# Performance work log

Measured on AMD Instinct MI355X. Metric: run time of the kernel, lower is better.

Reference implementation:

```python
import jax, jax.numpy as jnp
import numpy as np

D_THRESH = 0.5  # forward default d=0.5


def setup_inputs() -> dict:
    key = jax.random.key(0)
    C, P, D = 10, 1000, 1024
    # scale so pairwise distances (~sqrt(2D)*scale) straddle the 0.5 threshold
    feats = jax.random.normal(key, (C * P, D), dtype=jnp.float32) * 0.011
    ids_per_cls = jnp.arange(C * P, dtype=jnp.int64).reshape(C, P)
    return {"feats": feats, "ids_per_cls": ids_per_cls, "budget": 2000}


def reference(feats, ids_per_cls, budget):
    C, P = ids_per_cls.shape
    per_cls_budget = budget // C  # budget = int(budget / len(ids_per_cls_train))
    X = feats[ids_per_cls.reshape(-1)]  # [C*P, D] class-blocked representatives
    # pairwise euclidean distances (torch.cdist p=2), computed via gram trick
    sq = jnp.sum(X * X, axis=-1)  # [C*P]
    d2 = sq[:, None] + sq[None, :] - 2.0 * (X @ X.T)  # [C*P, C*P]
    dist = jnp.sqrt(jnp.maximum(d2, 0.0))
    # only count neighbors from OTHER classes (the per-class loop pops class i)
    cls = jnp.repeat(jnp.arange(C), P)  # [C*P]
    other = cls[:, None] != cls[None, :]  # [C*P, C*P] bool
    counts = jnp.sum((dist < D_THRESH) & other, axis=-1)  # [C*P] int
    counts = counts.reshape(C, P)
    # ascending sort by count, keep the `per_cls_budget` most-separated nodes
    order = jnp.argsort(counts, axis=-1)  # [C, P]
    sel = order[:, :per_cls_budget]  # [C, budget//C]
    ids_selected = jnp.take_along_axis(ids_per_cls, sel, axis=1).reshape(-1)
    return ids_selected, counts
```

## Files before the change

### kernel.cpp

```cpp
#include <hip/hip_runtime.h>

#define N_TOT 10000
#define CLS_P 1000
#define NC 10
#define D 1024

#define TM 128
#define DELTA 1.6e-5f
#define INV_SCALE2 4.8828125e-4f
#define ESC_CAP (1 << 22)
#define ESC_LOC 256
#define KCHUNKS (D / 32)
#define NTILE ((N_TOT + TM - 1) / TM)

typedef _Float16 f16x8 __attribute__((ext_vector_type(8)));
typedef float f32x4 __attribute__((ext_vector_type(4)));
typedef const __attribute__((address_space(1))) unsigned int* gptr_t;
typedef __attribute__((address_space(3))) unsigned int* lptr_t;

__global__ void zero_kernel(int* __restrict__ out, int n, int* __restrict__ esc_cnt) {
    int i = blockIdx.x * blockDim.x + threadIdx.x;
    if (i < n) out[i] = 0;
    if (i == 0) *esc_cnt = 0;
}

__global__ void prep_kernel(const float* __restrict__ feats, const int* __restrict__ ids,
                            unsigned short* __restrict__ Xh,
                            double* __restrict__ sqd, float* __restrict__ sqf) {
    int row = blockIdx.x;
    int id = ids[row];
    const float4* rp = (const float4*)(feats + (size_t)id * D);
    float4 v = rp[threadIdx.x];
    float f[4] = {v.x, v.y, v.z, v.w};
    ushort4 hv;
    unsigned short* hp = &hv.x;
    double s = 0.0;
    #pragma unroll
    for (int e = 0; e < 4; e++) {
        s += (double)f[e] * f[e];
        union { _Float16 h; unsigned short u; } cv;
        cv.h = (_Float16)(f[e] * 64.0f);
        hp[e] = cv.u;
    }
    *(ushort4*)(Xh + (size_t)row * D + threadIdx.x * 4) = hv;

    #pragma unroll
    for (int off = 32; off > 0; off >>= 1)
        s += __shfl_down(s, off, 64);
    __shared__ double wsum[4];
    int lane = threadIdx.x & 63, wv = threadIdx.x >> 6;
    if (lane == 0) wsum[wv] = s;
    __syncthreads();
    if (threadIdx.x == 0) {
        double t = wsum[0] + wsum[1] + wsum[2] + wsum[3];
        sqd[row] = t;
        sqf[row] = (float)t;
    }
}

__launch_bounds__(256, 3)
__global__ void count_kernel(const unsigned short* __restrict__ Xh,
                             const float* __restrict__ sqf,
                             int* __restrict__ counts,
                             int* __restrict__ esc_cnt, int2* __restrict__ esc_list) {
    int bid = blockIdx.y * gridDim.x + blockIdx.x;
    int it_t = 0, jt_t = 0;
    {
        int rem = bid, band = 0;
        while (true) {
            int h = NTILE - band * 8; if (h > 8) h = 8;
            int area = h * NTILE;
            if (rem < area) { it_t = band * 8 + rem % h; jt_t = rem / h; break; }
            rem -= area; band++;
        }
    }
    const int ib = it_t * TM, jb = jt_t * TM;
    if (jb < ib) return;

    {
        int ci0 = ib / CLS_P, ci1 = (ib + TM - 1) / CLS_P;
        int cj0 = jb / CLS_P, cj1 = (jb + TM - 1) / CLS_P;
        if (ci0 == ci1 && cj0 == cj1 && ci0 == cj0) return;
    }

    __shared__ unsigned short S[3 * 8192];
    __shared__ int cred_i[TM], cred_j[TM];
    __shared__ int esc_n, esc_base;
    __shared__ int2 esc_buf[ESC_LOC];

    const int tid = threadIdx.x;
    const int lane = tid & 63, w = tid >> 6;
    const int wi = (w & 1) * 64, wj = (w >> 1) * 64;
    const int quad = lane >> 4, col = lane & 15;

    if (tid == 0) esc_n = 0;

    const int warr = w >> 1;
    const int w01 = w & 1;
    const int rl0 = lane >> 2;
    const int slot = lane & 3;
    const int q = (slot - rl0 - (rl0 >> 2)) & 3;
    const int rowbase = warr ? jb : ib;

    const unsigned short* src[4];
    #pragma unroll
    for (int b = 0; b < 4; b++) {
        int grow = rowbase + b * 32 + w01 * 16 + rl0;
        if (grow > N_TOT - 1) grow = N_TOT - 1;
        src[b] = Xh + (size_t)grow * D + q * 8;
    }

#define STAGE(KC_, BUFBASE_)                                                     \
    {                                                                            \
        _Pragma("unroll")                                                        \
        for (int b = 0; b < 4; b++) {                                            \
            __builtin_amdgcn_global_load_lds(                                    \
                (gptr_t)(src[b] + (KC_) * 32),                                   \
                (lptr_t)((BUFBASE_) + warr * 4096 + b * 1024 + w01 * 512),       \
                16, 0, 0);                                                       \
        }                                                                        \
    }

#define FRAGS(BUFBASE_)                                                          \
    {                                                                            \
        _Pragma("unroll")                                                        \
        for (int t = 0; t < 4; t++) {                                            \
            int rA = wi + t * 16 + col;                                          \
            int sA = (quad + rA + (rA >> 2)) & 3;                                \
            ah[t] = *(const f16x8*)((BUFBASE_) + rA * 32 + sA * 8);              \
            int rB = wj + t * 16 + col;                                          \
            int sB = (quad + rB + (rB >> 2)) & 3;                                \
            bh[t] = *(const f16x8*)((BUFBASE_) + 4096 + rB * 32 + sB * 8);       \
        }                                                                        \
    }

#define MFMA16                                                                   \
    {                                                                            \
        _Pragma("unroll")                                                        \
        for (int it = 0; it < 4; it++)                                           \
            _Pragma("unroll")                                                    \
            for (int jt = 0; jt < 4; jt++)                                       \
                acc[it][jt] = __builtin_amdgcn_mfma_f32_16x16x32_f16(ah[it], bh[jt], acc[it][jt], 0, 0, 0); \
    }

    f32x4 acc[4][4];
    #pragma unroll
    for (int it = 0; it < 4; it++)
        #pragma unroll
        for (int jt = 0; jt < 4; jt++)
            acc[it][jt] = (f32x4){0.f, 0.f, 0.f, 0.f};

    f16x8 ah[4], bh[4];

    unsigned short* p0 = S;
    unsigned short* p1 = S + 8192;
    unsigned short* p2 = S + 16384;

    STAGE(0, p0);
    STAGE(1, p1);
    asm volatile("s_waitcnt vmcnt(4) lgkmcnt(0)\ns_barrier" ::: "memory");

    for (int kc = 0; kc < KCHUNKS; kc++) {
        if (kc + 2 < KCHUNKS) STAGE(kc + 2, p2);
        FRAGS(p0);
        if (kc + 2 < KCHUNKS) {
            asm volatile("s_waitcnt vmcnt(4) lgkmcnt(0)\ns_barrier" ::: "memory");
        } else {
            asm volatile("s_waitcnt vmcnt(0) lgkmcnt(0)\ns_barrier" ::: "memory");
        }
        MFMA16;
        unsigned short* t = p0; p0 = p1; p1 = p2; p2 = t;
    }

    if (tid < TM) { cred_i[tid] = 0; cred_j[tid] = 0; }
    __syncthreads();

    const float thr_lo = 0.25f - DELTA;
    const float thr_hi = 0.25f + DELTA;
    const bool diag = (ib == jb);

    float sqj[4];
    int clsj[4], jv[4], jidx[4];
    #pragma unroll
    for (int jt = 0; jt < 4; jt++) {
        int j = jb + wj + jt * 16 + col;
        jidx[jt] = j;
        jv[jt] = (j < N_TOT);
        sqj[jt] = jv[jt] ? sqf[j] : 0.f;
        clsj[jt] = j / CLS_P;
    }

    int cj[4] = {0, 0, 0, 0};

    #pragma unroll
    for (int it = 0; it < 4; it++) {
        #pragma unroll
        for (int r = 0; r < 4; r++) {
            int irow = wi + it * 16 + quad * 4 + r;
            int i = ib + irow;
            bool iv = (i < N_TOT);
            float sqi = iv ? sqf[i] : 0.f;
            int clsi = i / CLS_P;
            int ci = 0;
            #pragma unroll
            for (int jt = 0; jt < 4; jt++) {
                int j = jidx[jt];
                bool ok = iv && jv[jt] && (clsj[jt] != clsi) && (!diag || j > i);
                float d2 = sqi + sqj[jt] - acc[it][jt][r] * INV_SCALE2;
                bool in = ok && (d2 < thr_lo);
                bool esc = ok && !in && (d2 < thr_hi);
                ci += in ? 1 : 0;
                cj[jt] += in ? 1 : 0;
                if (esc) {
                    int k = atomicAdd(&esc_n, 1);
                    if (k < ESC_LOC) {
                        esc_buf[k] = make_int2(i, j);
                    } else {
                        int idx = atomicAdd(esc_cnt, 1);
                        if (idx < ESC_CAP) esc_list[idx] = make_int2(i, j);
                    }
                }
            }
            ci += __shfl_xor(ci, 1, 64);
            ci += __shfl_xor(ci, 2, 64);
            ci += __shfl_xor(ci, 4, 64);
            ci += __shfl_xor(ci, 8, 64);
            if (col == 0 && ci) atomicAdd(&cred_i[irow], ci);
        }
    }
    #pragma unroll
    for (int jt = 0; jt < 4; jt++) {
        int v = cj[jt];
        v += __shfl_xor(v, 16, 64);
        v += __shfl_xor(v, 32, 64);
        if (quad == 0 && v) atomicAdd(&cred_j[wj + jt * 16 + col], v);
    }
    __syncthreads();
    if (tid < TM) {
        int i = ib + tid;
        if (i < N_TOT && cred_i[tid]) atomicAdd(&counts[i], cred_i[tid]);
        int j = jb + tid;
        if (j < N_TOT && cred_j[tid]) atomicAdd(&counts[j], cred_j[tid]);
    }
    if (tid == 0) {
        int n = esc_n; if (n > ESC_LOC) n = ESC_LOC;
        esc_n = n;
        esc_base = atomicAdd(esc_cnt, n);
    }
    __syncthreads();
    for (int k = tid; k < esc_n; k += 256) {
        int idx = esc_base + k;
        if (idx < ESC_CAP) esc_list[idx] = esc_buf[k];
    }
}

__global__ void escalate_kernel(const float* __restrict__ feats, const int* __restrict__ ids,
                                const double* __restrict__ sqd,
                                const int* __restrict__ esc_cnt, const int2* __restrict__ esc_list,
                                int* __restrict__ counts) {
    int n = *esc_cnt;
    if (n > ESC_CAP) n = ESC_CAP;
    int lane = threadIdx.x & 63;
    int sub = lane >> 4;
    int l16 = lane & 15;
    int wglob = (blockIdx.x * blockDim.x + threadIdx.x) >> 6;
    int W = (gridDim.x * blockDim.x) >> 6;
    for (int p0 = wglob * 4; p0 < n; p0 += W * 4) {
        int p = p0 + sub;
        bool act = (p < n);
        int2 pr = act ? esc_list[p] : make_int2(0, 0);
        const float* xi = feats + (size_t)ids[pr.x] * D;
        const float* xj = feats + (size_t)ids[pr.y] * D;
        double s = 0.0;
        int k0 = l16 * 64;
        #pragma unroll
        for (int k = 0; k < 64; k += 4) {
            float4 a = *(const float4*)(xi + k0 + k);
            float4 b = *(const float4*)(xj + k0 + k);
            s += (double)a.x * b.x + (double)a.y * b.y + (double)a.z * b.z + (double)a.w * b.w;
        }
        s += __shfl_xor(s, 1, 64);
        s += __shfl_xor(s, 2, 64);
        s += __shfl_xor(s, 4, 64);
        s += __shfl_xor(s, 8, 64);
        if (act && l16 == 0) {
            double d2 = sqd[pr.x] + sqd[pr.y] - 2.0 * s;
            if (d2 < 0.25) {
                atomicAdd(&counts[pr.x], 1);
                atomicAdd(&counts[pr.y], 1);
            }
        }
    }
}

__global__ void sel_kernel(const int* __restrict__ counts, const int* __restrict__ ids,
                           int* __restrict__ out_ids, int pcb) {
    int c = blockIdx.x;
    __shared__ int lc[CLS_P];
    for (int p = threadIdx.x; p < CLS_P; p += blockDim.x)
        lc[p] = counts[c * CLS_P + p];
    __syncthreads();
    int p = threadIdx.x;
    if (p < CLS_P) {
        int cp = lc[p];
        int rank = 0;
        for (int qq = 0; qq < CLS_P; qq++) {
            int cq = lc[qq];
            rank += (cq < cp) || (cq == cp && qq < p);
        }
        if (rank < pcb)
            out_ids[c * pcb + rank] = ids[c * CLS_P + p];
    }
}

extern "C" void kernel_launch(void* const* d_in, const int* in_sizes, int n_in,
                              void* d_out, int out_size, void* d_ws, size_t ws_size,
                              hipStream_t stream) {
    const float* feats = (const float*)d_in[0];
    const int* ids = (const int*)d_in[1];
    int budget = out_size - N_TOT;
    int pcb = budget / NC;
    int* out = (int*)d_out;
    int* counts_out = out + NC * pcb;

    char* ws = (char*)d_ws;
    const size_t XH_OFF = 0;
    const size_t SQD_OFF = XH_OFF + (size_t)N_TOT * D * 2;
    const size_t SQF_OFF = SQD_OFF + (size_t)N_TOT * 8;
    const size_t ESCC_OFF = (SQF_OFF + (size_t)N_TOT * 4 + 63) & ~(size_t)63;
    const size_t ESCL_OFF = ESCC_OFF + 64;

    unsigned short* Xh = (unsigned short*)(ws + XH_OFF);
    double* sqd = (double*)(ws + SQD_OFF);
    float* sqf = (float*)(ws + SQF_OFF);
    int* esc_cnt = (int*)(ws + ESCC_OFF);
    int2* esc_list = (int2*)(ws + ESCL_OFF);

    zero_kernel<<<(out_size + 255) / 256, 256, 0, stream>>>(out, out_size, esc_cnt);
    prep_kernel<<<N_TOT, 256, 0, stream>>>(feats, ids, Xh, sqd, sqf);
    dim3 grid(NTILE, NTILE);
    count_kernel<<<grid, 256, 0, stream>>>(Xh, sqf, counts_out, esc_cnt, esc_list);
    escalate_kernel<<<4096, 256, 0, stream>>>(feats, ids, sqd, esc_cnt, esc_list, counts_out);
    sel_kernel<<<NC, 1024, 0, stream>>>(counts_out, ids, out, pcb);
}
```

Measured before the change: 362.7 us.

## Double-buffer MFMA fragments to overlap LDS reads with matrix math

Restructures the K-loop so LDS fragment loads for the next chunk go into a second register set while MFMAs run on the current set. The loop is unrolled by two and the per-step lgkmcnt(0) wait is dropped from the barrier. This is meant to hide LDS read latency behind MFMA work, at the cost of more VGPRs, which could lower occupancy. It also narrows the DELTA escalation band around the threshold, which sends fewer near-threshold pairs to the slow recheck path but risks misclassifying borderline distances.

```diff
diff --git a/kernel.cpp b/kernel.cpp
--- a/kernel.cpp
+++ b/kernel.cpp
@@ -6,7 +6,7 @@
 #define D 1024
 
 #define TM 128
-#define DELTA 1.6e-5f
+#define DELTA 1.35e-5f
 #define INV_SCALE2 4.8828125e-4f
 #define ESC_CAP (1 << 22)
 #define ESC_LOC 256
@@ -121,27 +121,30 @@
         }                                                                        \
     }
 
-#define FRAGS(BUFBASE_)                                                          \
+#define FRAGS_(AH, BH, BUFBASE_)                                                 \
     {                                                                            \
         _Pragma("unroll")                                                        \
         for (int t = 0; t < 4; t++) {                                            \
             int rA = wi + t * 16 + col;                                          \
             int sA = (quad + rA + (rA >> 2)) & 3;                                \
-            ah[t] = *(const f16x8*)((BUFBASE_) + rA * 32 + sA * 8);              \
+            AH[t] = *(const f16x8*)((BUFBASE_) + rA * 32 + sA * 8);              \
             int rB = wj + t * 16 + col;                                          \
             int sB = (quad + rB + (rB >> 2)) & 3;                                \
-            bh[t] = *(const f16x8*)((BUFBASE_) + 4096 + rB * 32 + sB * 8);       \
+            BH[t] = *(const f16x8*)((BUFBASE_) + 4096 + rB * 32 + sB * 8);       \
         }                                                                        \
     }
 
-#define MFMA16                                                                   \
+#define MFMA16_(AH, BH)                                                          \
     {                                                                            \
         _Pragma("unroll")                                                        \
         for (int it = 0; it < 4; it++)                                           \
             _Pragma("unroll")                                                    \
             for (int jt = 0; jt < 4; jt++)                                       \
-                acc[it][jt] = __builtin_amdgcn_mfma_f32_16x16x32_f16(ah[it], bh[jt], acc[it][jt], 0, 0, 0); \
-    }
+                acc[it][jt] = __builtin_amdgcn_mfma_f32_16x16x32_f16(AH[it], BH[jt], acc[it][jt], 0, 0, 0); \
+    }
+
+#define WAIT4_BAR asm volatile("s_waitcnt vmcnt(4)\ns_barrier" ::: "memory")
+#define WAIT0_BAR asm volatile("s_waitcnt vmcnt(0)\ns_barrier" ::: "memory")
 
     f32x4 acc[4][4];
     #pragma unroll
@@ -150,7 +153,7 @@
         for (int jt = 0; jt < 4; jt++)
             acc[it][jt] = (f32x4){0.f, 0.f, 0.f, 0.f};
 
-    f16x8 ah[4], bh[4];
+    f16x8 ah0[4], bh0[4], ah1[4], bh1[4];
 
     unsigned short* p0 = S;
     unsigned short* p1 = S + 8192;
@@ -158,19 +161,26 @@
 
     STAGE(0, p0);
     STAGE(1, p1);
-    asm volatile("s_waitcnt vmcnt(4) lgkmcnt(0)\ns_barrier" ::: "memory");
-
-    for (int kc = 0; kc < KCHUNKS; kc++) {
-        if (kc + 2 < KCHUNKS) STAGE(kc + 2, p2);
-        FRAGS(p0);
-        if (kc + 2 < KCHUNKS) {
-            asm volatile("s_waitcnt vmcnt(4) lgkmcnt(0)\ns_barrier" ::: "memory");
-        } else {
-            asm volatile("s_waitcnt vmcnt(0) lgkmcnt(0)\ns_barrier" ::: "memory");
-        }
-        MFMA16;
-        unsigned short* t = p0; p0 = p1; p1 = p2; p2 = t;
-    }
+    WAIT4_BAR;
+    FRAGS_(ah0, bh0, p0);
+
+    for (int kc = 0; kc < KCHUNKS - 2; kc += 2) {
+        STAGE(kc + 2, p2);
+        WAIT4_BAR;
+        FRAGS_(ah1, bh1, p1);
+        MFMA16_(ah0, bh0);
+        { unsigned short* t = p0; p0 = p1; p1 = p2; p2 = t; }
+
+        STAGE(kc + 3, p2);
+        WAIT4_BAR;
+        FRAGS_(ah0, bh0, p1);
+        MFMA16_(ah1, bh1);
+        { unsigned short* t = p0; p0 = p1; p1 = p2; p2 = t; }
+    }
+    WAIT0_BAR;
+    FRAGS_(ah1, bh1, p1);
+    MFMA16_(ah0, bh0);
+    MFMA16_(ah1, bh1);
 
     if (tid < TM) { cred_i[tid] = 0; cred_j[tid] = 0; }
     __syncthreads();
```

New measurement: 342.3 us. -5.6%, faster.

## Use 256x128 rectangular tiles with 4x8 MFMA per wave in count kernel

Applied to the files above, without the earlier changes.

Reworks the count kernel tiling from 128x128 square tiles to 256x128 tiles, with each wave owning 64 rows and all 128 columns, so each wave issues 32 MFMAs per k-chunk instead of 16. This raises arithmetic intensity per LDS fragment load, but it also uses more registers and LDS, so launch bounds drop to 2 blocks per SM. It removes the banded tile swizzle, narrows the escalation delta, enlarges the local escape buffer, and relaxes the lgkmcnt waits in the k-loop. Triangle skipping now works at a coarser granularity, and some tiles compute pairs that the j>i mask then discards.

```diff
diff --git a/kernel.cpp b/kernel.cpp
--- a/kernel.cpp
+++ b/kernel.cpp
@@ -5,13 +5,15 @@
 #define NC 10
 #define D 1024
 
-#define TM 128
-#define DELTA 1.6e-5f
+#define TMI 256
+#define TMJ 128
+#define DELTA 1.35e-5f
 #define INV_SCALE2 4.8828125e-4f
 #define ESC_CAP (1 << 22)
-#define ESC_LOC 256
+#define ESC_LOC 512
 #define KCHUNKS (D / 32)
-#define NTILE ((N_TOT + TM - 1) / TM)
+#define NTI ((N_TOT + TMI - 1) / TMI)
+#define NTJ ((N_TOT + TMJ - 1) / TMJ)
 
 typedef _Float16 f16x8 __attribute__((ext_vector_type(8)));
 typedef float f32x4 __attribute__((ext_vector_type(4)));
@@ -58,67 +60,67 @@
     }
 }
 
-__launch_bounds__(256, 3)
+__launch_bounds__(256, 2)
 __global__ void count_kernel(const unsigned short* __restrict__ Xh,
                              const float* __restrict__ sqf,
                              int* __restrict__ counts,
                              int* __restrict__ esc_cnt, int2* __restrict__ esc_list) {
-    int bid = blockIdx.y * gridDim.x + blockIdx.x;
-    int it_t = 0, jt_t = 0;
+    const int tjt = blockIdx.x;
+    const int tit = blockIdx.y;
+    if (tjt < 2 * tit) return;
+    const int ib = tit * TMI, jb = tjt * TMJ;
+
     {
-        int rem = bid, band = 0;
-        while (true) {
-            int h = NTILE - band * 8; if (h > 8) h = 8;
-            int area = h * NTILE;
-            if (rem < area) { it_t = band * 8 + rem % h; jt_t = rem / h; break; }
-            rem -= area; band++;
-        }
-    }
-    const int ib = it_t * TM, jb = jt_t * TM;
-    if (jb < ib) return;
-
-    {
-        int ci0 = ib / CLS_P, ci1 = (ib + TM - 1) / CLS_P;
-        int cj0 = jb / CLS_P, cj1 = (jb + TM - 1) / CLS_P;
+        int ihi = ib + TMI - 1; if (ihi > N_TOT - 1) ihi = N_TOT - 1;
+        int jhi = jb + TMJ - 1; if (jhi > N_TOT - 1) jhi = N_TOT - 1;
+        int ci0 = ib / CLS_P, ci1 = ihi / CLS_P;
+        int cj0 = jb / CLS_P, cj1 = jhi / CLS_P;
         if (ci0 == ci1 && cj0 == cj1 && ci0 == cj0) return;
     }
 
-    __shared__ unsigned short S[3 * 8192];
-    __shared__ int cred_i[TM], cred_j[TM];
+    __shared__ unsigned short S[3 * 12288];
+    __shared__ int cred_i[TMI], cred_j[TMJ];
     __shared__ int esc_n, esc_base;
     __shared__ int2 esc_buf[ESC_LOC];
 
     const int tid = threadIdx.x;
     const int lane = tid & 63, w = tid >> 6;
-    const int wi = (w & 1) * 64, wj = (w >> 1) * 64;
+    const int wi = w * 64;
     const int quad = lane >> 4, col = lane & 15;
 
     if (tid == 0) esc_n = 0;
 
-    const int warr = w >> 1;
-    const int w01 = w & 1;
     const int rl0 = lane >> 2;
     const int slot = lane & 3;
     const int q = (slot - rl0 - (rl0 >> 2)) & 3;
-    const int rowbase = warr ? jb : ib;
-
-    const unsigned short* src[4];
-    #pragma unroll
-    for (int b = 0; b < 4; b++) {
-        int grow = rowbase + b * 32 + w01 * 16 + rl0;
-        if (grow > N_TOT - 1) grow = N_TOT - 1;
-        src[b] = Xh + (size_t)grow * D + q * 8;
+
+    const unsigned short* srcA[4];
+    const unsigned short* srcB[2];
+    #pragma unroll
+    for (int c = 0; c < 4; c++) {
+        int r = ib + w * 64 + c * 16 + rl0;
+        if (r > N_TOT - 1) r = N_TOT - 1;
+        srcA[c] = Xh + (size_t)r * D + q * 8;
+    }
+    #pragma unroll
+    for (int c = 0; c < 2; c++) {
+        int r = jb + w * 32 + c * 16 + rl0;
+        if (r > N_TOT - 1) r = N_TOT - 1;
+        srcB[c] = Xh + (size_t)r * D + q * 8;
     }
 
 #define STAGE(KC_, BUFBASE_)                                                     \
     {                                                                            \
         _Pragma("unroll")                                                        \
-        for (int b = 0; b < 4; b++) {                                            \
+        for (int c = 0; c < 4; c++)                                              \
             __builtin_amdgcn_global_load_lds(                                    \
-                (gptr_t)(src[b] + (KC_) * 32),                                   \
-                (lptr_t)((BUFBASE_) + warr * 4096 + b * 1024 + w01 * 512),       \
-                16, 0, 0);                                                       \
-        }                                                                        \
+                (gptr_t)(srcA[c] + (KC_) * 32),                                  \
+                (lptr_t)((BUFBASE_) + w * 2048 + c * 512), 16, 0, 0);            \
+        _Pragma("unroll")                                                        \
+        for (int c = 0; c < 2; c++)                                              \
+            __builtin_amdgcn_global_load_lds(                                    \
+                (gptr_t)(srcB[c] + (KC_) * 32),                                  \
+                (lptr_t)((BUFBASE_) + 8192 + w * 1024 + c * 512), 16, 0, 0);     \
     }
 
 #define FRAGS(BUFBASE_)                                                          \
@@ -128,69 +130,72 @@
             int rA = wi + t * 16 + col;                                          \
             int sA = (quad + rA + (rA >> 2)) & 3;                                \
             ah[t] = *(const f16x8*)((BUFBASE_) + rA * 32 + sA * 8);              \
-            int rB = wj + t * 16 + col;                                          \
+        }                                                                        \
+        _Pragma("unroll")                                                        \
+        for (int u = 0; u < 8; u++) {                                            \
+            int rB = u * 16 + col;                                               \
             int sB = (quad + rB + (rB >> 2)) & 3;                                \
-            bh[t] = *(const f16x8*)((BUFBASE_) + 4096 + rB * 32 + sB * 8);       \
+            bh[u] = *(const f16x8*)((BUFBASE_) + 8192 + rB * 32 + sB * 8);       \
         }                                                                        \
     }
 
-#define MFMA16                                                                   \
+#define MFMA32                                                                   \
     {                                                                            \
         _Pragma("unroll")                                                        \
         for (int it = 0; it < 4; it++)                                           \
             _Pragma("unroll")                                                    \
-            for (int jt = 0; jt < 4; jt++)                                       \
+            for (int jt = 0; jt < 8; jt++)                                       \
                 acc[it][jt] = __builtin_amdgcn_mfma_f32_16x16x32_f16(ah[it], bh[jt], acc[it][jt], 0, 0, 0); \
     }
 
-    f32x4 acc[4][4];
+    f32x4 acc[4][8];
     #pragma unroll
     for (int it = 0; it < 4; it++)
         #pragma unroll
-        for (int jt = 0; jt < 4; jt++)
+        for (int jt = 0; jt < 8; jt++)
             acc[it][jt] = (f32x4){0.f, 0.f, 0.f, 0.f};
 
-    f16x8 ah[4], bh[4];
+    f16x8 ah[4], bh[8];
 
     unsigned short* p0 = S;
-    unsigned short* p1 = S + 8192;
-    unsigned short* p2 = S + 16384;
+    unsigned short* p1 = S + 12288;
+    unsigned short* p2 = S + 24576;
 
     STAGE(0, p0);
     STAGE(1, p1);
-    asm volatile("s_waitcnt vmcnt(4) lgkmcnt(0)\ns_barrier" ::: "memory");
+    asm volatile("s_waitcnt vmcnt(6) lgkmcnt(0)\ns_barrier" ::: "memory");
 
     for (int kc = 0; kc < KCHUNKS; kc++) {
         if (kc + 2 < KCHUNKS) STAGE(kc + 2, p2);
         FRAGS(p0);
         if (kc + 2 < KCHUNKS) {
-            asm volatile("s_waitcnt vmcnt(4) lgkmcnt(0)\ns_barrier" ::: "memory");
-        } else {
-            asm volatile("s_waitcnt vmcnt(0) lgkmcnt(0)\ns_barrier" ::: "memory");
-        }
-        MFMA16;
+            asm volatile("s_waitcnt vmcnt(6)\ns_barrier" ::: "memory");
+        } else if (kc + 1 < KCHUNKS) {
+            asm volatile("s_waitcnt vmcnt(0)\ns_barrier" ::: "memory");
+        }
+        MFMA32;
         unsigned short* t = p0; p0 = p1; p1 = p2; p2 = t;
     }
 
-    if (tid < TM) { cred_i[tid] = 0; cred_j[tid] = 0; }
+    cred_i[tid] = 0;
+    if (tid < TMJ) cred_j[tid] = 0;
     __syncthreads();
 
     const float thr_lo = 0.25f - DELTA;
     const float thr_hi = 0.25f + DELTA;
-    const bool diag = (ib == jb);
-
-    float sqj[4];
-    int clsj[4], jv[4], jidx[4];
-    #pragma unroll
-    for (int jt = 0; jt < 4; jt++) {
-        int j = jb + wj + jt * 16 + col;
+
+    float sqj[8];
+    int clsj[8], jv[8], jidx[8];
+    #pragma unroll
+    for (int jt = 0; jt < 8; jt++) {
+        int j = jb + jt * 16 + col;
         jidx[jt] = j;
         jv[jt] = (j < N_TOT);
         sqj[jt] = jv[jt] ? sqf[j] : 0.f;
         clsj[jt] = j / CLS_P;
     }
 
-    int cj[4] = {0, 0, 0, 0};
+    int cj[8] = {0, 0, 0, 0, 0, 0, 0, 0};
 
     #pragma unroll
     for (int it = 0; it < 4; it++) {
@@ -203,9 +208,9 @@
             int clsi = i / CLS_P;
             int ci = 0;
             #pragma unroll
-            for (int jt = 0; jt < 4; jt++) {
+            for (int jt = 0; jt < 8; jt++) {
                 int j = jidx[jt];
-                bool ok = iv && jv[jt] && (clsj[jt] != clsi) && (!diag || j > i);
+                bool ok = iv && jv[jt] && (clsj[jt] != clsi) && (j > i);
                 float d2 = sqi + sqj[jt] - acc[it][jt][r] * INV_SCALE2;
                 bool in = ok && (d2 < thr_lo);
                 bool esc = ok && !in && (d2 < thr_hi);
@@ -229,18 +234,20 @@
         }
     }
     #pragma unroll
-    for (int jt = 0; jt < 4; jt++) {
+    for (int jt = 0; jt < 8; jt++) {
         int v = cj[jt];
         v += __shfl_xor(v, 16, 64);
         v += __shfl_xor(v, 32, 64);
-        if (quad == 0 && v) atomicAdd(&cred_j[wj + jt * 16 + col], v);
-    }
-    __syncthreads();
-    if (tid < TM) {
+        if (quad == 0 && v) atomicAdd(&cred_j[jt * 16 + col], v);
+    }
+    __syncthreads();
+    {
         int i = ib + tid;
         if (i < N_TOT && cred_i[tid]) atomicAdd(&counts[i], cred_i[tid]);
-        int j = jb + tid;
-        if (j < N_TOT && cred_j[tid]) atomicAdd(&counts[j], cred_j[tid]);
+        if (tid < TMJ) {
+            int j = jb + tid;
+            if (j < N_TOT && cred_j[tid]) atomicAdd(&counts[j], cred_j[tid]);
+        }
     }
     if (tid == 0) {
         int n = esc_n; if (n > ESC_LOC) n = ESC_LOC;
@@ -338,7 +345,7 @@
 
     zero_kernel<<<(out_size + 255) / 256, 256, 0, stream>>>(out, out_size, esc_cnt);
     prep_kernel<<<N_TOT, 256, 0, stream>>>(feats, ids, Xh, sqd, sqf);
-    dim3 grid(NTILE, NTILE);
+    dim3 grid(NTJ, NTI);
     count_kernel<<<grid, 256, 0, stream>>>(Xh, sqf, counts_out, esc_cnt, esc_list);
     escalate_kernel<<<4096, 256, 0, stream>>>(feats, ids, sqd, esc_cnt, esc_list, counts_out);
     sel_kernel<<<NC, 1024, 0, stream>>>(counts_out, ids, out, pcb);
```

Measured after the change: 373.4 us. 3.0% more time.

## Fuse escalation into count kernel with single-wave 64x64 tiles

Applied to the files above, without the earlier changes.

Replaces the 256-thread, 128x128-tile count kernel with a one-wave, 64x64-tile kernel double-buffered in LDS without barriers. The escalation recheck of near-threshold pairs is now done inside the same kernel from a local buffer, with a slow per-thread fallback on overflow, so the global escalation list and the separate escalate kernel go away. It also narrows the ambiguity band (DELTA) and drops shared-memory count reduction in favour of direct global atomics. These changes cut a launch and global traffic, but each tile loses the 128x128 reuse, there are more global atomics, and the narrower band relies on FP16 error staying within it.

```diff
diff --git a/kernel.cpp b/kernel.cpp
--- a/kernel.cpp
+++ b/kernel.cpp
@@ -5,23 +5,21 @@
 #define NC 10
 #define D 1024
 
-#define TM 128
-#define DELTA 1.6e-5f
+#define TK 64
+#define DELTA 1.35e-5f
 #define INV_SCALE2 4.8828125e-4f
-#define ESC_CAP (1 << 22)
-#define ESC_LOC 256
+#define ESC_LOC 128
 #define KCHUNKS (D / 32)
-#define NTILE ((N_TOT + TM - 1) / TM)
+#define NT64 ((N_TOT + TK - 1) / TK)
 
 typedef _Float16 f16x8 __attribute__((ext_vector_type(8)));
 typedef float f32x4 __attribute__((ext_vector_type(4)));
 typedef const __attribute__((address_space(1))) unsigned int* gptr_t;
 typedef __attribute__((address_space(3))) unsigned int* lptr_t;
 
-__global__ void zero_kernel(int* __restrict__ out, int n, int* __restrict__ esc_cnt) {
+__global__ void zero_kernel(int* __restrict__ out, int n) {
     int i = blockIdx.x * blockDim.x + threadIdx.x;
     if (i < n) out[i] = 0;
-    if (i == 0) *esc_cnt = 0;
 }
 
 __global__ void prep_kernel(const float* __restrict__ feats, const int* __restrict__ ids,
@@ -58,89 +56,70 @@
     }
 }
 
-__launch_bounds__(256, 3)
+__launch_bounds__(64)
 __global__ void count_kernel(const unsigned short* __restrict__ Xh,
                              const float* __restrict__ sqf,
-                             int* __restrict__ counts,
-                             int* __restrict__ esc_cnt, int2* __restrict__ esc_list) {
-    int bid = blockIdx.y * gridDim.x + blockIdx.x;
-    int it_t = 0, jt_t = 0;
+                             const double* __restrict__ sqd,
+                             const float* __restrict__ feats,
+                             const int* __restrict__ ids,
+                             int* __restrict__ counts) {
+    int bid = blockIdx.y * NT64 + blockIdx.x;
+    int ti = 0, tj = 0;
     {
         int rem = bid, band = 0;
         while (true) {
-            int h = NTILE - band * 8; if (h > 8) h = 8;
-            int area = h * NTILE;
-            if (rem < area) { it_t = band * 8 + rem % h; jt_t = rem / h; break; }
+            int h = NT64 - band * 16; if (h > 16) h = 16;
+            int area = h * NT64;
+            if (rem < area) { ti = band * 16 + rem % h; tj = rem / h; break; }
             rem -= area; band++;
         }
     }
-    const int ib = it_t * TM, jb = jt_t * TM;
-    if (jb < ib) return;
+    if (tj < ti) return;
+    const int ib = ti * TK, jb = tj * TK;
 
     {
-        int ci0 = ib / CLS_P, ci1 = (ib + TM - 1) / CLS_P;
-        int cj0 = jb / CLS_P, cj1 = (jb + TM - 1) / CLS_P;
+        int ihi = ib + TK - 1; if (ihi > N_TOT - 1) ihi = N_TOT - 1;
+        int jhi = jb + TK - 1; if (jhi > N_TOT - 1) jhi = N_TOT - 1;
+        int ci0 = ib / CLS_P, ci1 = ihi / CLS_P;
+        int cj0 = jb / CLS_P, cj1 = jhi / CLS_P;
         if (ci0 == ci1 && cj0 == cj1 && ci0 == cj0) return;
     }
 
-    __shared__ unsigned short S[3 * 8192];
-    __shared__ int cred_i[TM], cred_j[TM];
-    __shared__ int esc_n, esc_base;
+    __shared__ unsigned short S[2 * 4096];
     __shared__ int2 esc_buf[ESC_LOC];
-
-    const int tid = threadIdx.x;
-    const int lane = tid & 63, w = tid >> 6;
-    const int wi = (w & 1) * 64, wj = (w >> 1) * 64;
+    __shared__ int esc_n;
+
+    const int lane = threadIdx.x;
     const int quad = lane >> 4, col = lane & 15;
 
-    if (tid == 0) esc_n = 0;
-
-    const int warr = w >> 1;
-    const int w01 = w & 1;
+    if (lane == 0) esc_n = 0;
+
     const int rl0 = lane >> 2;
     const int slot = lane & 3;
     const int q = (slot - rl0 - (rl0 >> 2)) & 3;
-    const int rowbase = warr ? jb : ib;
-
-    const unsigned short* src[4];
-    #pragma unroll
-    for (int b = 0; b < 4; b++) {
-        int grow = rowbase + b * 32 + w01 * 16 + rl0;
-        if (grow > N_TOT - 1) grow = N_TOT - 1;
-        src[b] = Xh + (size_t)grow * D + q * 8;
+
+    const unsigned short* srcA[4];
+    const unsigned short* srcB[4];
+    #pragma unroll
+    for (int c = 0; c < 4; c++) {
+        int rA = ib + c * 16 + rl0; if (rA > N_TOT - 1) rA = N_TOT - 1;
+        int rB = jb + c * 16 + rl0; if (rB > N_TOT - 1) rB = N_TOT - 1;
+        srcA[c] = Xh + (size_t)rA * D + q * 8;
+        srcB[c] = Xh + (size_t)rB * D + q * 8;
     }
 
 #define STAGE(KC_, BUFBASE_)                                                     \
     {                                                                            \
         _Pragma("unroll")                                                        \
-        for (int b = 0; b < 4; b++) {                                            \
+        for (int c = 0; c < 4; c++)                                              \
             __builtin_amdgcn_global_load_lds(                                    \
-                (gptr_t)(src[b] + (KC_) * 32),                                   \
-                (lptr_t)((BUFBASE_) + warr * 4096 + b * 1024 + w01 * 512),       \
-                16, 0, 0);                                                       \
-        }                                                                        \
-    }
-
-#define FRAGS(BUFBASE_)                                                          \
-    {                                                                            \
+                (gptr_t)(srcA[c] + (KC_) * 32),                                  \
+                (lptr_t)((BUFBASE_) + c * 512), 16, 0, 0);                       \
         _Pragma("unroll")                                                        \
-        for (int t = 0; t < 4; t++) {                                            \
-            int rA = wi + t * 16 + col;                                          \
-            int sA = (quad + rA + (rA >> 2)) & 3;                                \
-            ah[t] = *(const f16x8*)((BUFBASE_) + rA * 32 + sA * 8);              \
-            int rB = wj + t * 16 + col;                                          \
-            int sB = (quad + rB + (rB >> 2)) & 3;                                \
-            bh[t] = *(const f16x8*)((BUFBASE_) + 4096 + rB * 32 + sB * 8);       \
-        }                                                                        \
-    }
-
-#define MFMA16                                                                   \
-    {                                                                            \
-        _Pragma("unroll")                                                        \
-        for (int it = 0; it < 4; it++)                                           \
-            _Pragma("unroll")                                                    \
-            for (int jt = 0; jt < 4; jt++)                                       \
-                acc[it][jt] = __builtin_amdgcn_mfma_f32_16x16x32_f16(ah[it], bh[jt], acc[it][jt], 0, 0, 0); \
+        for (int c = 0; c < 4; c++)                                              \
+            __builtin_amdgcn_global_load_lds(                                    \
+                (gptr_t)(srcB[c] + (KC_) * 32),                                  \
+                (lptr_t)((BUFBASE_) + 2048 + c * 512), 16, 0, 0);                \
     }
 
     f32x4 acc[4][4];
@@ -152,38 +131,38 @@
 
     f16x8 ah[4], bh[4];
 
-    unsigned short* p0 = S;
-    unsigned short* p1 = S + 8192;
-    unsigned short* p2 = S + 16384;
-
-    STAGE(0, p0);
-    STAGE(1, p1);
-    asm volatile("s_waitcnt vmcnt(4) lgkmcnt(0)\ns_barrier" ::: "memory");
-
+    STAGE(0, S);
     for (int kc = 0; kc < KCHUNKS; kc++) {
-        if (kc + 2 < KCHUNKS) STAGE(kc + 2, p2);
-        FRAGS(p0);
-        if (kc + 2 < KCHUNKS) {
-            asm volatile("s_waitcnt vmcnt(4) lgkmcnt(0)\ns_barrier" ::: "memory");
+        unsigned short* cur = S + (kc & 1) * 4096;
+        unsigned short* nxt = S + ((kc + 1) & 1) * 4096;
+        if (kc + 1 < KCHUNKS) {
+            STAGE(kc + 1, nxt);
+            asm volatile("s_waitcnt vmcnt(8)" ::: "memory");
         } else {
-            asm volatile("s_waitcnt vmcnt(0) lgkmcnt(0)\ns_barrier" ::: "memory");
-        }
-        MFMA16;
-        unsigned short* t = p0; p0 = p1; p1 = p2; p2 = t;
-    }
-
-    if (tid < TM) { cred_i[tid] = 0; cred_j[tid] = 0; }
-    __syncthreads();
+            asm volatile("s_waitcnt vmcnt(0)" ::: "memory");
+        }
+        #pragma unroll
+        for (int t = 0; t < 4; t++) {
+            int rA = t * 16 + col;
+            int sA = (quad + rA + (rA >> 2)) & 3;
+            ah[t] = *(const f16x8*)(cur + rA * 32 + sA * 8);
+            bh[t] = *(const f16x8*)(cur + 2048 + rA * 32 + sA * 8);
+        }
+        #pragma unroll
+        for (int it = 0; it < 4; it++)
+            #pragma unroll
+            for (int jt = 0; jt < 4; jt++)
+                acc[it][jt] = __builtin_amdgcn_mfma_f32_16x16x32_f16(ah[it], bh[jt], acc[it][jt], 0, 0, 0);
+    }
 
     const float thr_lo = 0.25f - DELTA;
     const float thr_hi = 0.25f + DELTA;
-    const bool diag = (ib == jb);
 
     float sqj[4];
     int clsj[4], jv[4], jidx[4];
     #pragma unroll
     for (int jt = 0; jt < 4; jt++) {
-        int j = jb + wj + jt * 16 + col;
+        int j = jb + jt * 16 + col;
         jidx[jt] = j;
         jv[jt] = (j < N_TOT);
         sqj[jt] = jv[jt] ? sqf[j] : 0.f;
@@ -196,7 +175,7 @@
     for (int it = 0; it < 4; it++) {
         #pragma unroll
         for (int r = 0; r < 4; r++) {
-            int irow = wi + it * 16 + quad * 4 + r;
+            int irow = it * 16 + quad * 4 + r;
             int i = ib + irow;
             bool iv = (i < N_TOT);
             float sqi = iv ? sqf[i] : 0.f;
@@ -205,7 +184,7 @@
             #pragma unroll
             for (int jt = 0; jt < 4; jt++) {
                 int j = jidx[jt];
-                bool ok = iv && jv[jt] && (clsj[jt] != clsi) && (!diag || j > i);
+                bool ok = iv && jv[jt] && (clsj[jt] != clsi) && (j > i);
                 float d2 = sqi + sqj[jt] - acc[it][jt][r] * INV_SCALE2;
                 bool in = ok && (d2 < thr_lo);
                 bool esc = ok && !in && (d2 < thr_hi);
@@ -216,8 +195,14 @@
                     if (k < ESC_LOC) {
                         esc_buf[k] = make_int2(i, j);
                     } else {
-                        int idx = atomicAdd(esc_cnt, 1);
-                        if (idx < ESC_CAP) esc_list[idx] = make_int2(i, j);
+                        const float* xi = feats + (size_t)ids[i] * D;
+                        const float* xj = feats + (size_t)ids[j] * D;
+                        double s = 0.0;
+                        for (int kk = 0; kk < D; kk++) s += (double)xi[kk] * xj[kk];
+                        if (sqd[i] + sqd[j] - 2.0 * s < 0.25) {
+                            atomicAdd(&counts[i], 1);
+                            atomicAdd(&counts[j], 1);
+                        }
                     }
                 }
             }
@@ -225,7 +210,7 @@
             ci += __shfl_xor(ci, 2, 64);
             ci += __shfl_xor(ci, 4, 64);
             ci += __shfl_xor(ci, 8, 64);
-            if (col == 0 && ci) atomicAdd(&cred_i[irow], ci);
+            if (col == 0 && ci) atomicAdd(&counts[i], ci);
         }
     }
     #pragma unroll
@@ -233,42 +218,15 @@
         int v = cj[jt];
         v += __shfl_xor(v, 16, 64);
         v += __shfl_xor(v, 32, 64);
-        if (quad == 0 && v) atomicAdd(&cred_j[wj + jt * 16 + col], v);
-    }
-    __syncthreads();
-    if (tid < TM) {
-        int i = ib + tid;
-        if (i < N_TOT && cred_i[tid]) atomicAdd(&counts[i], cred_i[tid]);
-        int j = jb + tid;
-        if (j < N_TOT && cred_j[tid]) atomicAdd(&counts[j], cred_j[tid]);
-    }
-    if (tid == 0) {
-        int n = esc_n; if (n > ESC_LOC) n = ESC_LOC;
-        esc_n = n;
-        esc_base = atomicAdd(esc_cnt, n);
-    }
-    __syncthreads();
-    for (int k = tid; k < esc_n; k += 256) {
-        int idx = esc_base + k;
-        if (idx < ESC_CAP) esc_list[idx] = esc_buf[k];
-    }
-}
-
-__global__ void escalate_kernel(const float* __restrict__ feats, const int* __restrict__ ids,
-                                const double* __restrict__ sqd,
-                                const int* __restrict__ esc_cnt, const int2* __restrict__ esc_list,
-                                int* __restrict__ counts) {
-    int n = *esc_cnt;
-    if (n > ESC_CAP) n = ESC_CAP;
-    int lane = threadIdx.x & 63;
-    int sub = lane >> 4;
-    int l16 = lane & 15;
-    int wglob = (blockIdx.x * blockDim.x + threadIdx.x) >> 6;
-    int W = (gridDim.x * blockDim.x) >> 6;
-    for (int p0 = wglob * 4; p0 < n; p0 += W * 4) {
+        if (quad == 0 && v && jv[jt]) atomicAdd(&counts[jidx[jt]], v);
+    }
+
+    int n = esc_n; if (n > ESC_LOC) n = ESC_LOC;
+    const int sub = lane >> 4, l16 = lane & 15;
+    for (int p0 = 0; p0 < n; p0 += 4) {
         int p = p0 + sub;
         bool act = (p < n);
-        int2 pr = act ? esc_list[p] : make_int2(0, 0);
+        int2 pr = esc_buf[act ? p : 0];
         const float* xi = feats + (size_t)ids[pr.x] * D;
         const float* xj = feats + (size_t)ids[pr.y] * D;
         double s = 0.0;
@@ -327,19 +285,14 @@
     const size_t XH_OFF = 0;
     const size_t SQD_OFF = XH_OFF + (size_t)N_TOT * D * 2;
     const size_t SQF_OFF = SQD_OFF + (size_t)N_TOT * 8;
-    const size_t ESCC_OFF = (SQF_OFF + (size_t)N_TOT * 4 + 63) & ~(size_t)63;
-    const size_t ESCL_OFF = ESCC_OFF + 64;
 
     unsigned short* Xh = (unsigned short*)(ws + XH_OFF);
     double* sqd = (double*)(ws + SQD_OFF);
     float* sqf = (float*)(ws + SQF_OFF);
-    int* esc_cnt = (int*)(ws + ESCC_OFF);
-    int2* esc_list = (int2*)(ws + ESCL_OFF);
-
-    zero_kernel<<<(out_size + 255) / 256, 256, 0, stream>>>(out, out_size, esc_cnt);
+
+    zero_kernel<<<(out_size + 255) / 256, 256, 0, stream>>>(out, out_size);
     prep_kernel<<<N_TOT, 256, 0, stream>>>(feats, ids, Xh, sqd, sqf);
-    dim3 grid(NTILE, NTILE);
-    count_kernel<<<grid, 256, 0, stream>>>(Xh, sqf, counts_out, esc_cnt, esc_list);
-    escalate_kernel<<<4096, 256, 0, stream>>>(feats, ids, sqd, esc_cnt, esc_list, counts_out);
+    dim3 grid(NT64, NT64);
+    count_kernel<<<grid, 64, 0, stream>>>(Xh, sqf, sqd, feats, ids, counts_out);
     sel_kernel<<<NC, 1024, 0, stream>>>(counts_out, ids, out, pcb);
 }
```

After: 437.1 us. 1.21x slower.
